# Kernel optimization log

Hardware: AMD Instinct MI355X
Metric: run time of the kernel (lower is better)

## Reference

```python
import jax, jax.numpy as jnp
import numpy as np

# video grid and attention geometry (must match init_kwargs)
F_T, H_T, W_T = 4, 32, 32
K = 3                      # kernel_size (odd)
P = K // 2
T = F_T * H_T * W_T        # max_num_tokens = 4096
HEADS = 8
DIM_HEAD = 64
SCALE = DIM_HEAD ** -0.5
DIM = 512
INNER = HEADS * DIM_HEAD


def _build_window_indices():
    # flat token index grid, padded with sentinel T (out-of-range -> zero row after gather)
    idx = np.arange(T).reshape(F_T, H_T, W_T)
    padded = np.full((F_T + 2 * P, H_T + 2 * P, W_T + 2 * P), T, dtype=np.int64)
    padded[P:P + F_T, P:P + H_T, P:P + W_T] = idx
    # [T, K^3] neighborhood indices, kernel offsets in (kf, kh, kw) C-order (matches unfoldNd)
    win = np.lib.stride_tricks.sliding_window_view(padded, (K, K, K)).reshape(T, K ** 3)
    # causal: mask keys whose flat index is strictly in the future of the query
    causal = np.arange(T)[:, None] < win
    causal = np.concatenate([np.zeros((T, 1), dtype=bool), causal], axis=1)  # BOS column never masked
    return jnp.asarray(win), jnp.asarray(causal)

WIN_IDX, CAUSAL_MASK = _build_window_indices()


def setup_inputs() -> dict:
    key = jax.random.key(0)
    k0, k1, k2, k3 = jax.random.split(key, 4)
    n = T  # 1 BOS + (T-1) video tokens; padding logic pads body to exactly T tokens
    x = jax.random.normal(k0, (2, n, DIM), dtype=jnp.float32)
    Wq = jax.random.normal(k1, (DIM, INNER), dtype=jnp.float32) * (DIM ** -0.5)
    Wkv = jax.random.normal(k2, (DIM, 2 * INNER), dtype=jnp.float32) * (DIM ** -0.5)
    Wo = jax.random.normal(k3, (INNER, DIM), dtype=jnp.float32) * (INNER ** -0.5)
    bo = jnp.zeros((DIM,), dtype=jnp.float32)
    return {"x": x, "Wq": Wq, "Wkv": Wkv, "Wo": Wo, "bo": bo}


def _split_heads(t, b):
    # [b, n, h*d] -> [(b*h), n, d]
    n = t.shape[1]
    return t.reshape(b, n, HEADS, DIM_HEAD).transpose(0, 2, 1, 3).reshape(b * HEADS, n, DIM_HEAD)


def reference(x, Wq, Wkv, Wo, bo):
    b, n, _ = x.shape
    tpf = H_T * W_T
    padding = tpf - (n - 1) % tpf  # pads body tokens to a multiple of tokens_per_frame
    x = jnp.pad(x, ((0, 0), (0, padding), (0, 0)))
    q = x @ Wq
    k, v = jnp.split(x @ Wkv, 2, axis=-1)
    q, k, v = (_split_heads(t, b) for t in (q, k, v))
    bh = b * HEADS
    q = q[:, 1:] * SCALE            # drop BOS query; [bh, T, d]
    bos_v = v[:, :1]                # BOS attends only to itself -> its value passes through
    k_bos, k = k[:, :1], k[:, 1:]
    v_bos, v = v[:, :1], v[:, 1:]
    # gather K^3 3D neighborhoods; sentinel index T maps to a zero row
    zero_row = jnp.zeros((bh, 1, DIM_HEAD), dtype=k.dtype)
    k_nb = jnp.concatenate([k, zero_row], axis=1)[:, WIN_IDX]   # [bh, T, K^3, d]
    v_nb = jnp.concatenate([v, zero_row], axis=1)[:, WIN_IDX]
    # prepend global BOS key/value to every window
    k_nb = jnp.concatenate([jnp.broadcast_to(k_bos[:, :, None], (bh, T, 1, DIM_HEAD)), k_nb], axis=2)
    v_nb = jnp.concatenate([jnp.broadcast_to(v_bos[:, :, None], (bh, T, 1, DIM_HEAD)), v_nb], axis=2)
    sim = jnp.einsum('bid,bijd->bij', q, k_nb)                  # [bh, T, K^3+1]
    sim = jnp.where(CAUSAL_MASK[None], -jnp.finfo(sim.dtype).max, sim)
    attn = jax.nn.softmax(sim, axis=-1)
    out = jnp.einsum('bij,bijd->bid', attn, v_nb)               # [bh, T, d]
    out = jnp.concatenate([bos_v, out], axis=1)                 # [bh, T+1, d]
    np_tok = out.shape[1]
    out = out.reshape(b, HEADS, np_tok, DIM_HEAD).transpose(0, 2, 1, 3).reshape(b, np_tok, INNER)
    return (out @ Wo + bo)[:, :n]
```

## Files before the change

kernel.cpp:

```cpp
#include <hip/hip_runtime.h>


#define T_TOK   4096
#define DIM     512
#define NQKV    1536

typedef unsigned short u16;
typedef unsigned int   u32;
typedef unsigned long long u64;
typedef __attribute__((ext_vector_type(8))) short short8;
typedef __attribute__((ext_vector_type(4))) float f32x4;

__device__ __forceinline__ u16 f2bf(float f) {
    u32 u = __float_as_uint(f);
    return (u16)((u + 0x7fffu + ((u >> 16) & 1u)) >> 16);
}
__device__ __forceinline__ float b2f(u16 u) {
    return __uint_as_float(((u32)u) << 16);
}

__device__ __forceinline__ void gload_lds16(const void* g, void* l) {
    __builtin_amdgcn_global_load_lds(
        (const __attribute__((address_space(1))) void*)g,
        (__attribute__((address_space(3))) void*)l, 16, 0, 0);
}

__global__ void cast_all_kernel(const float4* __restrict__ x,
                                const float* __restrict__ Wq, const float* __restrict__ Wkv,
                                const float* __restrict__ Wo,
                                u16* __restrict__ xb, u16* __restrict__ Wt,
                                u16* __restrict__ Wot) {
    __shared__ float S[64 * 65];
    int blk = blockIdx.x;
    int tid = threadIdx.x;
    if (blk < 4096) {
        int i = blk * 256 + tid;
        float4 v = x[i];
        u64 pack = (u64)f2bf(v.x) | ((u64)f2bf(v.y) << 16) |
                   ((u64)f2bf(v.z) << 32) | ((u64)f2bf(v.w) << 48);
        ((u64*)xb)[i] = pack;
        return;
    }
    int isWo = blk >= 4288;
    int tIdx = isWo ? (blk - 4288) : (blk - 4096);
    int tn = tIdx >> 3, tk = tIdx & 7;
    #pragma unroll
    for (int p = 0; p < 16; ++p) {
        int kl = p * 4 + (tid >> 6), nl = tid & 63;
        int gk = tk * 64 + kl, gn = tn * 64 + nl;
        float v;
        if (isWo)            v = Wo[gk * 512 + gn];
        else if (gn < 512)   v = Wq[gk * 512 + gn];
        else                 v = Wkv[gk * 1024 + (gn - 512)];
        S[kl * 65 + nl] = v;
    }
    __syncthreads();
    u16* dst = isWo ? Wot : Wt;
    #pragma unroll
    for (int p = 0; p < 16; ++p) {
        int nl = p * 4 + (tid >> 6), kl = tid & 63;
        dst[(size_t)(tn * 64 + nl) * 512 + tk * 64 + kl] = f2bf(S[kl * 65 + nl]);
    }
}

template <int BM, int BN, int MODE>
__global__ __launch_bounds__(256)
void gemm_nt(const u16* __restrict__ A, const u16* __restrict__ B,
             void* __restrict__ Cv, const float* __restrict__ bias,
             int lda, int ldb, int ldc) {
    constexpr int K = 512, BK = 32, KSTEPS = K / BK;
    constexpr int ACH = BM * 4;
    constexpr int NCH = (BM + BN) * 4;
    constexpr int NLD = NCH / 256;
    constexpr int ABYTES = BM * 64;
    constexpr int HALF = (BM + BN) * 64;
    constexpr int MI = BM / 32, NJ = BN / 32;
    __shared__ __align__(16) char lds[2 * HALF];
    const int tid  = threadIdx.x;
    const int lane = tid & 63, wave = tid >> 6;
    const int quad = lane >> 4, mrow = lane & 15;
    const int wm = wave >> 1, wn = wave & 1;
    const int bm = blockIdx.y, bn = blockIdx.x;

    const char* gptr[NLD];
    char*       lptr[NLD];
    #pragma unroll
    for (int it = 0; it < NLD; ++it) {
        int c   = it * 256 + tid;
        int inB = (c >= ACH);
        int a   = inB ? c - ACH : c;
        int r   = a >> 2;
        int kc  = ((a & 3) - (r >> 1)) & 3;
        int row = (inB ? bn * BN : bm * BM) + r;
        const u16* base = inB ? B : A;
        int ld = inB ? ldb : lda;
        gptr[it] = (const char*)(base + (size_t)row * ld + kc * 8);
        lptr[it] = (char*)lds + (it * 256 + wave * 64) * 16;
    }
    const char* aLds[MI];
    const char* bLds[NJ];
    #pragma unroll
    for (int i = 0; i < MI; ++i) {
        int ra = wm * (BM / 2) + i * 16 + mrow;
        aLds[i] = lds + (ra * 4 + ((quad + (ra >> 1)) & 3)) * 16;
    }
    #pragma unroll
    for (int j = 0; j < NJ; ++j) {
        int rb = wn * (BN / 2) + j * 16 + mrow;
        bLds[j] = lds + ABYTES + (rb * 4 + ((quad + (rb >> 1)) & 3)) * 16;
    }

    f32x4 acc[MI][NJ] = {};
    #pragma unroll
    for (int it = 0; it < NLD; ++it)
        gload_lds16(gptr[it], lptr[it]);

    #pragma unroll
    for (int ks = 0; ks < KSTEPS; ++ks) {
        const int cur = ks & 1;
        if (ks + 1 < KSTEPS) {
            #pragma unroll
            for (int it = 0; it < NLD; ++it)
                gload_lds16(gptr[it] + 2 * (ks + 1) * BK, lptr[it] + (cur ^ 1) * HALF);
            asm volatile("s_waitcnt vmcnt(%0)" :: "i"(NLD) : "memory");
        } else {
            asm volatile("s_waitcnt vmcnt(0)" ::: "memory");
        }
        asm volatile("s_barrier" ::: "memory");

        short8 af[MI], bf[NJ];
        #pragma unroll
        for (int i = 0; i < MI; ++i) af[i] = *(const short8*)(aLds[i] + cur * HALF);
        #pragma unroll
        for (int j = 0; j < NJ; ++j) bf[j] = *(const short8*)(bLds[j] + cur * HALF);
        #pragma unroll
        for (int i = 0; i < MI; ++i)
            #pragma unroll
            for (int j = 0; j < NJ; ++j)
                acc[i][j] = __builtin_amdgcn_mfma_f32_16x16x32_bf16(af[i], bf[j], acc[i][j], 0, 0, 0);
        asm volatile("s_waitcnt lgkmcnt(0)" ::: "memory");
        asm volatile("s_barrier" ::: "memory");
    }

    #pragma unroll
    for (int i = 0; i < MI; ++i) {
        #pragma unroll
        for (int j = 0; j < NJ; ++j) {
            int colg = bn * BN + wn * (BN / 2) + j * 16 + mrow;
            #pragma unroll
            for (int r = 0; r < 4; ++r) {
                int rowg = bm * BM + wm * (BM / 2) + i * 16 + quad * 4 + r;
                if (MODE == 0) {
                    ((u16*)Cv)[(size_t)rowg * ldc + colg] = f2bf(acc[i][j][r]);
                } else {
                    ((float*)Cv)[(size_t)rowg * ldc + colg] = acc[i][j][r] + bias[colg];
                }
            }
        }
    }
}

__global__ __launch_bounds__(256)
void attn_kernel(const u16* __restrict__ QKV, u16* __restrict__ O) {
    const int wid  = blockIdx.x * 4 + (threadIdx.x >> 6);
    const int lane = threadIdx.x & 63;
    const int b  = wid >> 14;
    const int hp = (wid >> 12) & 3;
    const int ti = wid & 4095;
    const int h0 = hp * 2, h1 = h0 + 1;
    const size_t baseQ = (size_t)b * T_TOK * NQKV;
    const size_t baseO = (size_t)b * T_TOK * DIM;

    if (ti == 0) {
        O[baseO + h0 * 64 + lane] = QKV[baseQ + 1024 + h0 * 64 + lane];
        O[baseO + h1 * 64 + lane] = QKV[baseQ + 1024 + h1 * 64 + lane];
        return;
    }
    const int t = ti - 1;
    const int f = t >> 10, hh = (t >> 5) & 31, ww = t & 31;

    const int j = lane >> 2, g = lane & 3;
    int jm1 = j - 1;
    int dh9 = ((jm1 * 11) >> 5) - 1;
    int dw9 = jm1 - (dh9 + 1) * 3 - 1;
    int df = (j >= 1 && j <= 9) ? -1 : 0;
    int dh = (j >= 1 && j <= 9) ? dh9 : ((j >= 10 && j <= 12) ? -1 : 0);
    int dw = (j >= 1 && j <= 9) ? dw9 :
             ((j >= 10 && j <= 12) ? (j - 11) : ((j == 13) ? -1 : 0));
    int nf = f + df, nh = hh + dh, nw = ww + dw;
    int valid = (nf >= 0) && ((unsigned)nh < 32u) && ((unsigned)nw < 32u)
                && (j >= 1) && (j <= 14);
    int p = valid ? (t + 1 + df * 1024 + dh * 32 + dw) : 0;
    int score_on = valid || (j == 0);

    const u16* qbase = QKV + baseQ + (size_t)(t + 1) * NQKV + g * 16;
    const u16* kbase = QKV + baseQ + (size_t)p * NQKV + 512 + g * 16;
    short8 q0a = *(const short8*)(qbase + h0 * 64);
    short8 q0b = *(const short8*)(qbase + h0 * 64 + 8);
    short8 q1a = *(const short8*)(qbase + h1 * 64);
    short8 q1b = *(const short8*)(qbase + h1 * 64 + 8);
    short8 k0a = *(const short8*)(kbase + h0 * 64);
    short8 k0b = *(const short8*)(kbase + h0 * 64 + 8);
    short8 k1a = *(const short8*)(kbase + h1 * 64);
    short8 k1b = *(const short8*)(kbase + h1 * 64 + 8);
    float s0 = 0.f, s1 = 0.f;
    #pragma unroll
    for (int i = 0; i < 8; ++i) {
        s0 = fmaf(b2f((u16)q0a[i]), b2f((u16)k0a[i]), s0);
        s1 = fmaf(b2f((u16)q1a[i]), b2f((u16)k1a[i]), s1);
        s0 = fmaf(b2f((u16)q0b[i]), b2f((u16)k0b[i]), s0);
        s1 = fmaf(b2f((u16)q1b[i]), b2f((u16)k1b[i]), s1);
    }
    s0 += __shfl_xor(s0, 1);  s1 += __shfl_xor(s1, 1);
    s0 += __shfl_xor(s0, 2);  s1 += __shfl_xor(s1, 2);
    s0 *= 0.125f;             s1 *= 0.125f;
    s0 = score_on ? s0 : -3.0e38f;
    s1 = score_on ? s1 : -3.0e38f;

    float m0 = s0, m1 = s1;
    #pragma unroll
    for (int off = 4; off <= 32; off <<= 1) {
        m0 = fmaxf(m0, __shfl_xor(m0, off));
        m1 = fmaxf(m1, __shfl_xor(m1, off));
    }
    float pe0 = __expf(s0 - m0), pe1 = __expf(s1 - m1);
    float l0 = pe0, l1 = pe1;
    #pragma unroll
    for (int off = 4; off <= 32; off <<= 1) {
        l0 += __shfl_xor(l0, off);
        l1 += __shfl_xor(l1, off);
    }
    float pen0 = pe0 * __frcp_rn(l0);
    float pen1 = pe1 * __frcp_rn(l1);
    u32 voff = (u32)p * 3072u;

    float acc0 = 0.f, acc1 = 0.f;
    const char* vb0 = (const char*)(QKV + baseQ + 1024 + h0 * 64 + lane);
    const char* vb1 = (const char*)(QKV + baseQ + 1024 + h1 * 64 + lane);
    #pragma unroll
    for (int jj = 0; jj < 15; ++jj) {
        u32 o = (u32)__builtin_amdgcn_readlane((int)voff, jj * 4);
        float pj0 = __uint_as_float(
                      (u32)__builtin_amdgcn_readlane((int)__float_as_uint(pen0), jj * 4));
        float pj1 = __uint_as_float(
                      (u32)__builtin_amdgcn_readlane((int)__float_as_uint(pen1), jj * 4));
        float v0 = b2f(*(const u16*)(vb0 + o));
        float v1 = b2f(*(const u16*)(vb1 + o));
        acc0 = fmaf(pj0, v0, acc0);
        acc1 = fmaf(pj1, v1, acc1);
    }
    O[baseO + (size_t)ti * DIM + h0 * 64 + lane] = f2bf(acc0);
    O[baseO + (size_t)ti * DIM + h1 * 64 + lane] = f2bf(acc1);
}

extern "C" void kernel_launch(void* const* d_in, const int* in_sizes, int n_in,
                              void* d_out, int out_size, void* d_ws, size_t ws_size,
                              hipStream_t stream) {
    const float* x   = (const float*)d_in[0];
    const float* Wq  = (const float*)d_in[1];
    const float* Wkv = (const float*)d_in[2];
    const float* Wo  = (const float*)d_in[3];
    const float* bo  = (const float*)d_in[4];
    float* out = (float*)d_out;
    char* ws = (char*)d_ws;

    u16* xb  = (u16*)(ws + 0);
    u16* Wt  = (u16*)(ws + 8388608);
    u16* Wot = (u16*)(ws + 9961472);
    u16* QKV = (u16*)(ws + 10485760);
    u16* O   = (u16*)(ws + 0);

    cast_all_kernel<<<dim3(4352), dim3(256), 0, stream>>>(
        (const float4*)x, Wq, Wkv, Wo, xb, Wt, Wot);
    gemm_nt<128, 128, 0><<<dim3(12, 64), dim3(256), 0, stream>>>(
        xb, Wt, (void*)QKV, nullptr, 512, 512, 1536);
    attn_kernel<<<dim3(8192), dim3(256), 0, stream>>>(QKV, O);
    gemm_nt<128, 64, 1><<<dim3(8, 64), dim3(256), 0, stream>>>(
        O, Wot, (void*)out, bo, 512, 512, 512);
}
```

Baseline: 134.8 us.

## Replace 4-wave GEMM with single-wave 64x64 tile kernel using 3-stage prefetch

Both projection GEMMs now use a one-wave-per-block kernel with 64x64 output tiles. Each wave loads its own tiles into LDS, so the block-wide barriers go away. Loads are issued two K-steps ahead, and the buffer refill happens after the MFMAs. The grid grows from 768 to 3072 blocks for QKV and from 512 to 1024 for the output projection, giving more parallelism. In exchange, each block gets less tile reuse, so there is more global and LDS traffic per flop.

```diff
diff --git a/kernel.cpp b/kernel.cpp
--- a/kernel.cpp
+++ b/kernel.cpp
@@ -63,93 +63,86 @@
     }
 }
 
-template <int BM, int BN, int MODE>
-__global__ __launch_bounds__(256)
-void gemm_nt(const u16* __restrict__ A, const u16* __restrict__ B,
+template <int MODE>
+__global__ __launch_bounds__(64)
+void gemm_1w(const u16* __restrict__ A, const u16* __restrict__ B,
              void* __restrict__ Cv, const float* __restrict__ bias,
              int lda, int ldb, int ldc) {
     constexpr int K = 512, BK = 32, KSTEPS = K / BK;
-    constexpr int ACH = BM * 4;
-    constexpr int NCH = (BM + BN) * 4;
-    constexpr int NLD = NCH / 256;
-    constexpr int ABYTES = BM * 64;
-    constexpr int HALF = (BM + BN) * 64;
-    constexpr int MI = BM / 32, NJ = BN / 32;
+    constexpr int NLD = 8;
+    constexpr int ABYTES = 64 * 64;
+    constexpr int HALF = 8192;
     __shared__ __align__(16) char lds[2 * HALF];
-    const int tid  = threadIdx.x;
-    const int lane = tid & 63, wave = tid >> 6;
+    const int lane = threadIdx.x & 63;
     const int quad = lane >> 4, mrow = lane & 15;
-    const int wm = wave >> 1, wn = wave & 1;
     const int bm = blockIdx.y, bn = blockIdx.x;
 
     const char* gptr[NLD];
     char*       lptr[NLD];
     #pragma unroll
     for (int it = 0; it < NLD; ++it) {
-        int c   = it * 256 + tid;
-        int inB = (c >= ACH);
-        int a   = inB ? c - ACH : c;
+        int c   = it * 64 + lane;
+        int inB = (c >= 256);
+        int a   = inB ? c - 256 : c;
         int r   = a >> 2;
         int kc  = ((a & 3) - (r >> 1)) & 3;
-        int row = (inB ? bn * BN : bm * BM) + r;
+        int row = (inB ? bn : bm) * 64 + r;
         const u16* base = inB ? B : A;
         int ld = inB ? ldb : lda;
         gptr[it] = (const char*)(base + (size_t)row * ld + kc * 8);
-        lptr[it] = (char*)lds + (it * 256 + wave * 64) * 16;
-    }
-    const char* aLds[MI];
-    const char* bLds[NJ];
-    #pragma unroll
-    for (int i = 0; i < MI; ++i) {
-        int ra = wm * (BM / 2) + i * 16 + mrow;
+        lptr[it] = (char*)lds + it * 1024;
+    }
+    const char* aLds[4];
+    const char* bLds[4];
+    #pragma unroll
+    for (int i = 0; i < 4; ++i) {
+        int ra = i * 16 + mrow;
         aLds[i] = lds + (ra * 4 + ((quad + (ra >> 1)) & 3)) * 16;
-    }
-    #pragma unroll
-    for (int j = 0; j < NJ; ++j) {
-        int rb = wn * (BN / 2) + j * 16 + mrow;
-        bLds[j] = lds + ABYTES + (rb * 4 + ((quad + (rb >> 1)) & 3)) * 16;
-    }
-
-    f32x4 acc[MI][NJ] = {};
+        bLds[i] = lds + ABYTES + (ra * 4 + ((ra >> 1) + quad & 3)) * 16;
+    }
+
+    f32x4 acc[4][4] = {};
     #pragma unroll
     for (int it = 0; it < NLD; ++it)
         gload_lds16(gptr[it], lptr[it]);
+    #pragma unroll
+    for (int it = 0; it < NLD; ++it)
+        gload_lds16(gptr[it] + 2 * BK, lptr[it] + HALF);
 
     #pragma unroll
     for (int ks = 0; ks < KSTEPS; ++ks) {
-        const int cur = ks & 1;
+        const int cur = (ks & 1) * HALF;
         if (ks + 1 < KSTEPS) {
-            #pragma unroll
-            for (int it = 0; it < NLD; ++it)
-                gload_lds16(gptr[it] + 2 * (ks + 1) * BK, lptr[it] + (cur ^ 1) * HALF);
             asm volatile("s_waitcnt vmcnt(%0)" :: "i"(NLD) : "memory");
         } else {
             asm volatile("s_waitcnt vmcnt(0)" ::: "memory");
         }
-        asm volatile("s_barrier" ::: "memory");
-
-        short8 af[MI], bf[NJ];
-        #pragma unroll
-        for (int i = 0; i < MI; ++i) af[i] = *(const short8*)(aLds[i] + cur * HALF);
-        #pragma unroll
-        for (int j = 0; j < NJ; ++j) bf[j] = *(const short8*)(bLds[j] + cur * HALF);
-        #pragma unroll
-        for (int i = 0; i < MI; ++i)
+        short8 af[4], bf[4];
+        #pragma unroll
+        for (int i = 0; i < 4; ++i) af[i] = *(const short8*)(aLds[i] + cur);
+        #pragma unroll
+        for (int j = 0; j < 4; ++j) bf[j] = *(const short8*)(bLds[j] + cur);
+        asm volatile("s_waitcnt lgkmcnt(0)" ::: "memory");
+        #pragma unroll
+        for (int i = 0; i < 4; ++i)
             #pragma unroll
-            for (int j = 0; j < NJ; ++j)
+            for (int j = 0; j < 4; ++j)
                 acc[i][j] = __builtin_amdgcn_mfma_f32_16x16x32_bf16(af[i], bf[j], acc[i][j], 0, 0, 0);
-        asm volatile("s_waitcnt lgkmcnt(0)" ::: "memory");
-        asm volatile("s_barrier" ::: "memory");
-    }
-
-    #pragma unroll
-    for (int i = 0; i < MI; ++i) {
-        #pragma unroll
-        for (int j = 0; j < NJ; ++j) {
-            int colg = bn * BN + wn * (BN / 2) + j * 16 + mrow;
+        if (ks + 2 < KSTEPS) {
+            #pragma unroll
+            for (int it = 0; it < NLD; ++it)
+                gload_lds16(gptr[it] + 2 * (ks + 2) * BK, lptr[it] + cur);
+        }
+    }
+
+    #pragma unroll
+    for (int i = 0; i < 4; ++i) {
+        #pragma unroll
+        for (int j = 0; j < 4; ++j) {
+            int colg = bn * 64 + j * 16 + mrow;
             #pragma unroll
             for (int r = 0; r < 4; ++r) {
-                int rowg = bm * BM + wm * (BM / 2) + i * 16 + quad * 4 + r;
+                int rowg = bm * 64 + i * 16 + quad * 4 + r;
                 if (MODE == 0) {
                     ((u16*)Cv)[(size_t)rowg * ldc + colg] = f2bf(acc[i][j][r]);
                 } else {
@@ -272,9 +265,9 @@
 
     cast_all_kernel<<<dim3(4352), dim3(256), 0, stream>>>(
         (const float4*)x, Wq, Wkv, Wo, xb, Wt, Wot);
-    gemm_nt<128, 128, 0><<<dim3(12, 64), dim3(256), 0, stream>>>(
+    gemm_1w<0><<<dim3(24, 128), dim3(64), 0, stream>>>(
         xb, Wt, (void*)QKV, nullptr, 512, 512, 1536);
     attn_kernel<<<dim3(8192), dim3(256), 0, stream>>>(QKV, O);
-    gemm_nt<128, 64, 1><<<dim3(8, 64), dim3(256), 0, stream>>>(
+    gemm_1w<1><<<dim3(8, 128), dim3(64), 0, stream>>>(
         O, Wot, (void*)out, bo, 512, 512, 512);
 }
```

After: 149.1 us. 10.6% more time.
